# Kernel tuning notes

Measured on AMD Instinct MI355X. Metric: run time of the kernel, lower is better.

## Reference

```python
import jax, jax.numpy as jnp
import numpy as np

B, N, C = 4096, 20, 512
S_VIEWS = 8
N_VIEWS = 20


def setup_inputs() -> dict:
    key = jax.random.key(0)
    k1, k2, k3, k4 = jax.random.split(key, 4)
    F0 = jax.random.normal(k1, (B, N, C), dtype=jnp.float32)
    vertices0 = jax.random.normal(k2, (B, N, 3), dtype=jnp.float32)
    W1 = jax.random.normal(k3, (C, 256), dtype=jnp.float32) * 0.04
    b1 = jnp.zeros((256,), dtype=jnp.float32)
    W2 = jax.random.normal(k4, (256, 40), dtype=jnp.float32) * 0.06
    b2 = jnp.zeros((40,), dtype=jnp.float32)
    return {"F0": F0, "vertices0": vertices0, "W1": W1, "b1": b1, "W2": W2, "b2": b2, "k": 8}


def _cls(x, W1, b1, W2, b2):
    # Linear(512,256) -> LeakyReLU(0.2) -> Linear(256,40)
    h = x @ W1 + b1
    h = jnp.where(h > 0, h, 0.2 * h)
    return h @ W2 + b2


def reference(F0, vertices0, W1, b1, W2, b2, k):
    # F0: [B, N, C]; vertices0: [B, N, 3]
    pooled_F = jnp.sum(F0, axis=1) / N_VIEWS                 # [B, C]
    pred = jnp.argmax(_cls(pooled_F, W1, b1, W2, b2), -1)    # [B] predicted class per sample
    score = _cls(F0, W1, b1, W2, b2)                         # [B, N, 40]
    # score[arange(B), :, pred] -> per-view score of the predicted class
    score_F = jnp.take_along_axis(score, pred[:, None, None], axis=2)[..., 0]  # [B, N]
    _, idx = jax.lax.top_k(score_F, S_VIEWS)                 # [B, S]
    F_new = jnp.take_along_axis(F0, idx[:, :, None], axis=1)            # [B, S, C]
    vertices_new = jnp.take_along_axis(vertices0, idx[:, :, None], axis=1)  # [B, S, 3]
    return (F_new, score, vertices_new)
```

## Files before the change

kernel.cpp:

```cpp
#include <hip/hip_runtime.h>
#include <cstdint>

#define BB 4096
#define NV 20
#define CC 512
#define HH 256
#define NC 40
#define SV 8
#define GG 3
#define TAU 2e-4f

typedef short short8 __attribute__((ext_vector_type(8)));
typedef float f32x4 __attribute__((ext_vector_type(4)));
typedef unsigned short ushort4v __attribute__((ext_vector_type(4)));

__device__ __forceinline__ unsigned short f2bf(float x) {
    unsigned u = __float_as_uint(x);
    unsigned r = (u + 0x7FFFu + ((u >> 16) & 1u)) >> 16;
    return (unsigned short)r;
}
__device__ __forceinline__ float bf2f(unsigned short h) {
    return __uint_as_float(((unsigned)h) << 16);
}

#define MFMA16(A, B, C) __builtin_amdgcn_mfma_f32_16x16x32_bf16(A, B, C, 0, 0, 0)
#define BC8(x) __builtin_bit_cast(short8, x)

__global__ void w1pack_kernel(const float* __restrict__ W1,
                              unsigned short* __restrict__ w1fh,
                              unsigned short* __restrict__ w1fl) {
    int e = blockIdx.x * 256 + threadIdx.x;
    int j3 = e & 7, kq = (e >> 3) & 3, n = (e >> 5) & 255, ks = e >> 13;
    int k = ks * 32 + kq * 8 + j3;
    float x = W1[k * HH + n];
    unsigned short h = f2bf(x);
    w1fh[e] = h;
    w1fl[e] = f2bf(x - bf2f(h));
}

__global__ void w2pack_kernel(const float* __restrict__ W2,
                              unsigned short* __restrict__ w2fh,
                              unsigned short* __restrict__ w2fl) {
    int e = blockIdx.x * 256 + threadIdx.x;
    int j3 = e & 7, kq = (e >> 3) & 3;
    int t = e >> 5;
    int n = t % 48, ks = t / 48;
    int k = ks * 32 + kq * 8 + j3;
    float x = (n < NC) ? W2[k * NC + n] : 0.f;
    unsigned short h = f2bf(x);
    w2fh[e] = h;
    w2fl[e] = f2bf(x - bf2f(h));
}

__global__ __launch_bounds__(256, 3) void fused_kernel(
    const float* __restrict__ F0, const float* __restrict__ V0,
    const float* __restrict__ W1, const float* __restrict__ b1,
    const float* __restrict__ W2, const float* __restrict__ b2,
    const unsigned short* __restrict__ w1fh, const unsigned short* __restrict__ w1fl,
    const unsigned short* __restrict__ w2fh, const unsigned short* __restrict__ w2fl,
    int* __restrict__ rflag, int* __restrict__ rpred,
    float* __restrict__ outF, float* __restrict__ outS, float* __restrict__ outV)
{
    const int blk = blockIdx.x;
    const int j = threadIdx.x;
    const int L = j & 63, wq = j >> 6, l15 = L & 15, kq = L >> 4;

    __shared__ __align__(16) char lds[46944];
    __shared__ int idx8[GG][SV];

    unsigned short* Ahi0 = (unsigned short*)lds;
    unsigned short* Alo0 = Ahi0 + 64 * 72;
    unsigned short* Ahi1 = (unsigned short*)(lds + 18432);
    unsigned short* Alo1 = Ahi1 + 64 * 72;
    unsigned short* Hhi  = (unsigned short*)lds;
    unsigned short* Hlo  = Hhi + 32 * 264;
    float*  Sc      = (float*)(lds + 36864);

    f32x4 acc[4][4];
#pragma unroll
    for (int mt = 0; mt < 4; ++mt)
#pragma unroll
        for (int nt = 0; nt < 4; ++nt) acc[mt][nt] = (f32x4){0.f, 0.f, 0.f, 0.f};

    const float4* srcp[4];
    int ldst[4];
    bool sval[4];
#pragma unroll
    for (int i = 0; i < 4; ++i) {
        int f = j + 256 * i;
        int row = f >> 4, k4 = f & 15;
        sval[i] = (row < 60);
        int bi = (row >= 40) ? 2 : (row >= 20) ? 1 : 0;
        int r = row - 20 * bi;
        int batch = blk * GG + bi; if (batch > BB - 1) batch = BB - 1;
        srcp[i] = (const float4*)(F0 + ((size_t)batch * NV + r) * CC) + k4;
        ldst[i] = row * 72 + k4 * 4;
    }

    float4 rv[4];
    auto STAGE_LOAD = [&](int kc) {
#pragma unroll
        for (int i = 0; i < 4; ++i)
            if (sval[i]) rv[i] = srcp[i][kc * 16];
    };
    auto STAGE_CONVERT = [&](unsigned short* __restrict__ Ah,
                             unsigned short* __restrict__ Al) {
#pragma unroll
        for (int i = 0; i < 4; ++i) {
            ushort4v hv = {0, 0, 0, 0}, lv = {0, 0, 0, 0};
            if (sval[i]) {
                float4 x = rv[i];
                hv.x = f2bf(x.x); lv.x = f2bf(x.x - bf2f(hv.x));
                hv.y = f2bf(x.y); lv.y = f2bf(x.y - bf2f(hv.y));
                hv.z = f2bf(x.z); lv.z = f2bf(x.z - bf2f(hv.z));
                hv.w = f2bf(x.w); lv.w = f2bf(x.w - bf2f(hv.w));
            }
            *(ushort4v*)&Ah[ldst[i]] = hv;
            *(ushort4v*)&Al[ldst[i]] = lv;
        }
    };

    const uint4* Bh = (const uint4*)w1fh;
    const uint4* Bl = (const uint4*)w1fl;

    STAGE_LOAD(0);
    STAGE_CONVERT(Ahi0, Alo0);
    STAGE_LOAD(1);
    __syncthreads();

    unsigned short *Ahc = Ahi0, *Alc = Alo0, *Ahn = Ahi1, *Aln = Alo1;
    for (int kc = 0; kc < 8; ++kc) {
        if (kc < 7) {
            STAGE_CONVERT(Ahn, Aln);
            if (kc < 6) STAGE_LOAD(kc + 2);
        }
#pragma unroll
        for (int ks_l = 0; ks_l < 2; ++ks_l) {
            int ks = kc * 2 + ks_l;
            uint4 bh[4], bl[4];
#pragma unroll
            for (int nt = 0; nt < 4; ++nt) {
                int bi1 = (ks * 256 + wq * 64 + nt * 16 + l15) * 4 + kq;
                bh[nt] = Bh[bi1]; bl[nt] = Bl[bi1];
            }
#pragma unroll
            for (int mt = 0; mt < 4; ++mt) {
                int off = (mt * 16 + l15) * 72 + ks_l * 32 + kq * 8;
                short8 Ah = BC8(*(const uint4*)&Ahc[off]);
                short8 Al = BC8(*(const uint4*)&Alc[off]);
#pragma unroll
                for (int nt = 0; nt < 4; ++nt) {
                    short8 Bhv = BC8(bh[nt]), Blv = BC8(bl[nt]);
                    acc[mt][nt] = MFMA16(Ah, Bhv, acc[mt][nt]);
                    acc[mt][nt] = MFMA16(Ah, Blv, acc[mt][nt]);
                    acc[mt][nt] = MFMA16(Al, Bhv, acc[mt][nt]);
                }
            }
        }
        __syncthreads();
        unsigned short* t;
        t = Ahc; Ahc = Ahn; Ahn = t;
        t = Alc; Alc = Aln; Aln = t;
    }

    const uint4* B2h = (const uint4*)w2fh;
    const uint4* B2l = (const uint4*)w2fl;
#pragma unroll
    for (int p = 0; p < 2; ++p) {
        __syncthreads();
#pragma unroll
        for (int mt2 = 0; mt2 < 2; ++mt2) {
            int mt = 2 * p + mt2;
            bool skip = (p == 1 && mt2 == 1 && kq == 3);
#pragma unroll
            for (int nt = 0; nt < 4; ++nt) {
                int col = wq * 64 + nt * 16 + l15;
                float bc = b1[col];
#pragma unroll
                for (int reg = 0; reg < 4; ++reg) {
                    int hb = mt2 * 16 + kq * 4 + reg;
                    float h = acc[mt][nt][reg] + bc;
                    h = (h > 0.f) ? h : 0.2f * h;
                    if (!skip) {
                        unsigned short hh = f2bf(h);
                        Hhi[hb * 264 + col] = hh;
                        Hlo[hb * 264 + col] = f2bf(h - bf2f(hh));
                    }
                }
            }
        }
        if (p == 1) {
#pragma unroll
            for (int nt = 0; nt < 4; ++nt) {
                int col = wq * 64 + nt * 16 + l15;
                float p0 = 0.f, p1 = 0.f, p2 = 0.f;
#pragma unroll
                for (int mt = 0; mt < 4; ++mt)
#pragma unroll
                    for (int reg = 0; reg < 4; ++reg) {
                        int g = mt * 16 + kq * 4 + reg;
                        float v = acc[mt][nt][reg];
                        p0 += (g < 20) ? v : 0.f;
                        p1 += (g >= 20 && g < 40) ? v : 0.f;
                        p2 += (g >= 40 && g < 60) ? v : 0.f;
                    }
                p0 += __shfl_xor(p0, 16); p0 += __shfl_xor(p0, 32);
                p1 += __shfl_xor(p1, 16); p1 += __shfl_xor(p1, 32);
                p2 += __shfl_xor(p2, 16); p2 += __shfl_xor(p2, 32);
                if (kq < 3) {
                    float s = (kq == 0) ? p0 : (kq == 1) ? p1 : p2;
                    float h = s * (1.0f / NV) + b1[col];
                    h = (h > 0.f) ? h : 0.2f * h;
                    unsigned short hh = f2bf(h);
                    Hhi[(28 + kq) * 264 + col] = hh;
                    Hlo[(28 + kq) * 264 + col] = f2bf(h - bf2f(hh));
                } else {
                    Hhi[31 * 264 + col] = 0;
                    Hlo[31 * 264 + col] = 0;
                }
            }
        }
        __syncthreads();

        if (wq < 3) {
            f32x4 sacc[2];
            sacc[0] = (f32x4){0.f, 0.f, 0.f, 0.f};
            sacc[1] = (f32x4){0.f, 0.f, 0.f, 0.f};
            for (int ks2 = 0; ks2 < 8; ++ks2) {
                int bi2 = (ks2 * 48 + wq * 16 + l15) * 4 + kq;
                short8 Bhv = BC8(B2h[bi2]), Blv = BC8(B2l[bi2]);
#pragma unroll
                for (int tt = 0; tt < 2; ++tt) {
                    int off = (tt * 16 + l15) * 264 + ks2 * 32 + kq * 8;
                    short8 Ah2 = BC8(*(const uint4*)&Hhi[off]);
                    short8 Al2 = BC8(*(const uint4*)&Hlo[off]);
                    sacc[tt] = MFMA16(Ah2, Bhv, sacc[tt]);
                    sacc[tt] = MFMA16(Ah2, Blv, sacc[tt]);
                    sacc[tt] = MFMA16(Al2, Bhv, sacc[tt]);
                }
            }
            int cls = wq * 16 + l15;
            if (cls < NC) {
                float bc2 = b2[cls];
#pragma unroll
                for (int tt = 0; tt < 2; ++tt)
#pragma unroll
                    for (int reg = 0; reg < 4; ++reg) {
                        int lm = 32 * p + tt * 16 + kq * 4 + reg;
                        float sv = sacc[tt][reg] + bc2;
                        if (lm < 60) {
                            int bi = (lm >= 40) ? 2 : (lm >= 20) ? 1 : 0;
                            int r = lm - 20 * bi;
                            Sc[bi * 840 + r * NC + cls] = sv;
                        } else if (lm < 63) {
                            Sc[(lm - 60) * 840 + NV * NC + cls] = sv;
                        }
                    }
            }
        }
    }
    __syncthreads();

    if (j < GG) {
        const float* sp = &Sc[j * 840 + NV * NC];
        int p = 0;
        float m1 = sp[0];
        for (int c = 1; c < NC; ++c)
            if (sp[c] > m1) { m1 = sp[c]; p = c; }
        float m2 = -1e30f;
        for (int c = 0; c < NC; ++c)
            if (c != p && sp[c] > m2) m2 = sp[c];
        int f0 = (m1 - m2 < TAU) ? 1 : 0;

        float v[NV];
#pragma unroll
        for (int n = 0; n < NV; ++n) v[n] = Sc[j * 840 + n * NC + p];
        int ord[9];
        float vals[9];
        unsigned taken = 0;
#pragma unroll
        for (int s = 0; s < 9; ++s) {
            int bi = 0;
            float bv = -1e30f;
#pragma unroll
            for (int n = 0; n < NV; ++n)
                if (!((taken >> n) & 1u) && v[n] > bv) { bv = v[n]; bi = n; }
            taken |= 1u << bi;
            ord[s] = bi;
            vals[s] = bv;
        }
        int fix = 0;
#pragma unroll
        for (int s = 0; s < 8; ++s)
            if (vals[s] - vals[s + 1] < TAU) fix = 1;
#pragma unroll
        for (int s = 0; s < SV; ++s) idx8[j][s] = ord[s];

        int batch = blk * GG + j; if (batch > BB - 1) batch = BB - 1;
        rflag[batch] = f0 ? 1 : (fix ? 2 : 0);
        rpred[batch] = p;
    }
    __syncthreads();

    for (int t = j; t < GG * NV * NC; t += 256) {
        int bi = t / 800, o = t - bi * 800;
        int batch = blk * GG + bi; if (batch > BB - 1) batch = BB - 1;
        outS[(size_t)batch * (NV * NC) + o] = Sc[bi * 840 + o];
    }

    for (int t = j; t < GG * SV * (CC / 4); t += 256) {
        int bi = t >> 10;
        int s = (t >> 7) & 7;
        int t4 = t & 127;
        int batch = blk * GG + bi; if (batch > BB - 1) batch = BB - 1;
        int row = idx8[bi][s];
        const float4* src = (const float4*)(F0 + ((size_t)batch * NV + row) * CC);
        float4* dst = (float4*)(outF + ((size_t)batch * SV + s) * CC);
        dst[t4] = src[t4];
    }

    if (j < GG * SV * 3) {
        int bi = j / 24, o = j - bi * 24;
        int s = o / 3, d = o - s * 3;
        int batch = blk * GG + bi; if (batch > BB - 1) batch = BB - 1;
        outV[((size_t)batch * SV + s) * 3 + d] =
            V0[((size_t)batch * NV + idx8[bi][s]) * 3 + d];
    }
}

__global__ __launch_bounds__(256) void rescue_kernel(
    const float* __restrict__ F0, const float* __restrict__ V0,
    const float* __restrict__ W1, const float* __restrict__ b1,
    const float* __restrict__ W2, const float* __restrict__ b2,
    const int* __restrict__ rflag, const int* __restrict__ rpred,
    float* __restrict__ outF, float* __restrict__ outV)
{
    const int b = blockIdx.x;
    const int flag = rflag[b];
    if (flag == 0) return;

    const int j = threadIdx.x;
    const int L = j & 63, wq = j >> 6;

    __shared__ __align__(16) float Xf[NV * CC];
    __shared__ double pooledD[CC];
    __shared__ double Dbuf[HH];
    __shared__ double Sd[NC];
    __shared__ double part[NV][4];
    __shared__ double SFdS[NV];
    __shared__ int predSh;
    __shared__ int idxs[SV];

    const float* Xb = F0 + (size_t)b * (NV * CC);
    for (int t = j; t < NV * CC / 4; t += 256)
        ((float4*)Xf)[t] = ((const float4*)Xb)[t];
    __syncthreads();

    if (flag == 1) {
        for (int c = j; c < CC; c += 256) {
            double s = 0.0;
            for (int r = 0; r < NV; ++r) s += (double)Xf[r * CC + c];
            pooledD[c] = s / (double)NV;
        }
        __syncthreads();
        double a = 0.0;
        for (int c = 0; c < CC; ++c) a += pooledD[c] * (double)W1[c * HH + j];
        double h = a + (double)b1[j];
        h = (h > 0.0) ? h : 0.2 * h;
        Dbuf[j] = h;
        __syncthreads();
        if (j < NC) {
            double s = 0.0;
            for (int k = 0; k < HH; ++k) s += Dbuf[k] * (double)W2[k * NC + j];
            Sd[j] = s + (double)b2[j];
        }
        __syncthreads();
        if (j == 0) {
            int p = 0;
            double m = Sd[0];
            for (int c = 1; c < NC; ++c)
                if (Sd[c] > m) { m = Sd[c]; p = c; }
            predSh = p;
        }
        __syncthreads();
    } else {
        if (j == 0) predSh = rpred[b];
        __syncthreads();
    }
    const int p = predSh;

    const double b1d = (double)b1[j];
    const double w2jp = (double)W2[j * NC + p];
#pragma unroll
    for (int half = 0; half < 2; ++half) {
        double a[10];
#pragma unroll
        for (int r = 0; r < 10; ++r) a[r] = 0.0;
        for (int c = 0; c < CC; c += 4) {
            double w0 = (double)W1[(c + 0) * HH + j];
            double w1v = (double)W1[(c + 1) * HH + j];
            double w2v = (double)W1[(c + 2) * HH + j];
            double w3v = (double)W1[(c + 3) * HH + j];
#pragma unroll
            for (int r = 0; r < 10; ++r) {
                const float4 x = *(const float4*)&Xf[(half * 10 + r) * CC + c];
                a[r] += (double)x.x * w0;
                a[r] += (double)x.y * w1v;
                a[r] += (double)x.z * w2v;
                a[r] += (double)x.w * w3v;
            }
        }
#pragma unroll
        for (int r = 0; r < 10; ++r) {
            double h = a[r] + b1d;
            h = (h > 0.0) ? h : 0.2 * h;
            double val = h * w2jp;
#pragma unroll
            for (int off = 32; off >= 1; off >>= 1)
                val += __shfl_xor(val, off);
            if (L == 0) part[half * 10 + r][wq] = val;
        }
    }
    __syncthreads();
    if (j < NV)
        SFdS[j] = part[j][0] + part[j][1] + part[j][2] + part[j][3]
                + (double)b2[p];
    __syncthreads();
    if (j == 0) {
        unsigned taken = 0;
        for (int s = 0; s < SV; ++s) {
            int bsel = 0;
            double bv = -1e300;
            for (int n = 0; n < NV; ++n)
                if (!((taken >> n) & 1u) && SFdS[n] > bv) { bv = SFdS[n]; bsel = n; }
            taken |= 1u << bsel;
            idxs[s] = bsel;
        }
    }
    __syncthreads();

    for (int t = j; t < SV * (CC / 4); t += 256) {
        int s = t >> 7, t4 = t & 127;
        int row = idxs[s];
        ((float4*)(outF + ((size_t)b * SV + s) * CC))[t4] =
            ((const float4*)(F0 + ((size_t)b * NV + row) * CC))[t4];
    }
    if (j < SV * 3) {
        int s = j / 3, d = j - s * 3;
        outV[((size_t)b * SV + s) * 3 + d] =
            V0[((size_t)b * NV + idxs[s]) * 3 + d];
    }
}

extern "C" void kernel_launch(void* const* d_in, const int* in_sizes, int n_in,
                              void* d_out, int out_size, void* d_ws, size_t ws_size,
                              hipStream_t stream) {
    const float* F0 = (const float*)d_in[0];
    const float* V0 = (const float*)d_in[1];
    const float* W1 = (const float*)d_in[2];
    const float* b1 = (const float*)d_in[3];
    const float* W2 = (const float*)d_in[4];
    const float* b2 = (const float*)d_in[5];

    char* ws = (char*)d_ws;
    unsigned short* w1fh = (unsigned short*)ws;
    unsigned short* w1fl = (unsigned short*)(ws + 262144);
    unsigned short* w2fh = (unsigned short*)(ws + 524288);
    unsigned short* w2fl = (unsigned short*)(ws + 548864);
    int* rflag = (int*)(ws + 573440);
    int* rpred = (int*)(ws + 589824);

    float* out = (float*)d_out;
    float* outF = out;
    float* outS = out + (size_t)BB * SV * CC;
    float* outV = outS + (size_t)BB * NV * NC;

    w1pack_kernel<<<512, 256, 0, stream>>>(W1, w1fh, w1fl);
    w2pack_kernel<<<48, 256, 0, stream>>>(W2, w2fh, w2fl);
    fused_kernel<<<(BB + GG - 1) / GG, 256, 0, stream>>>(
        F0, V0, W1, b1, W2, b2, w1fh, w1fl, w2fh, w2fl, rflag, rpred,
        outF, outS, outV);
    rescue_kernel<<<BB, 256, 0, stream>>>(
        F0, V0, W1, b1, W2, b2, rflag, rpred, outF, outV);
}
```

Before: 464.8 us.

## Load A operands directly to registers, merge pack kernels, compact rescue worklist

The fused kernel no longer stages F0 tiles through double-buffered LDS. Each lane now loads its own A fragment from global memory and splits it into bf16 hi/lo in registers, which removes the per-chunk barriers and LDS traffic but adds uncoalesced loads and redundant conversion across waves. The two weight-pack kernels are merged into one launch that also resets a counter. Flagged batches are appended to an atomic worklist, so the rescue kernel runs 256 blocks over that list instead of launching one block per batch.

```diff
diff --git a/kernel.cpp b/kernel.cpp
--- a/kernel.cpp
+++ b/kernel.cpp
@@ -12,7 +12,7 @@
 
 typedef short short8 __attribute__((ext_vector_type(8)));
 typedef float f32x4 __attribute__((ext_vector_type(4)));
-typedef unsigned short ushort4v __attribute__((ext_vector_type(4)));
+typedef unsigned short ushort8v __attribute__((ext_vector_type(8)));
 
 __device__ __forceinline__ unsigned short f2bf(float x) {
     unsigned u = __float_as_uint(x);
@@ -26,55 +26,53 @@
 #define MFMA16(A, B, C) __builtin_amdgcn_mfma_f32_16x16x32_bf16(A, B, C, 0, 0, 0)
 #define BC8(x) __builtin_bit_cast(short8, x)
 
-__global__ void w1pack_kernel(const float* __restrict__ W1,
-                              unsigned short* __restrict__ w1fh,
-                              unsigned short* __restrict__ w1fl) {
+__global__ void pack_kernel(const float* __restrict__ W1,
+                            const float* __restrict__ W2,
+                            unsigned short* __restrict__ w1fh,
+                            unsigned short* __restrict__ w1fl,
+                            unsigned short* __restrict__ w2fh,
+                            unsigned short* __restrict__ w2fl,
+                            int* __restrict__ wcount) {
     int e = blockIdx.x * 256 + threadIdx.x;
-    int j3 = e & 7, kq = (e >> 3) & 3, n = (e >> 5) & 255, ks = e >> 13;
-    int k = ks * 32 + kq * 8 + j3;
-    float x = W1[k * HH + n];
-    unsigned short h = f2bf(x);
-    w1fh[e] = h;
-    w1fl[e] = f2bf(x - bf2f(h));
-}
-
-__global__ void w2pack_kernel(const float* __restrict__ W2,
-                              unsigned short* __restrict__ w2fh,
-                              unsigned short* __restrict__ w2fl) {
-    int e = blockIdx.x * 256 + threadIdx.x;
-    int j3 = e & 7, kq = (e >> 3) & 3;
-    int t = e >> 5;
-    int n = t % 48, ks = t / 48;
-    int k = ks * 32 + kq * 8 + j3;
-    float x = (n < NC) ? W2[k * NC + n] : 0.f;
-    unsigned short h = f2bf(x);
-    w2fh[e] = h;
-    w2fl[e] = f2bf(x - bf2f(h));
+    if (e == 0) *wcount = 0;
+    {
+        int j3 = e & 7, kq = (e >> 3) & 3, n = (e >> 5) & 255, ks = e >> 13;
+        int k = ks * 32 + kq * 8 + j3;
+        float x = W1[k * HH + n];
+        unsigned short h = f2bf(x);
+        w1fh[e] = h;
+        w1fl[e] = f2bf(x - bf2f(h));
+    }
+    if (e < 12288) {
+        int j3 = e & 7, kq = (e >> 3) & 3;
+        int t = e >> 5;
+        int n = t % 48, ks = t / 48;
+        int k = ks * 32 + kq * 8 + j3;
+        float x = (n < NC) ? W2[k * NC + n] : 0.f;
+        unsigned short h = f2bf(x);
+        w2fh[e] = h;
+        w2fl[e] = f2bf(x - bf2f(h));
+    }
 }
 
 __global__ __launch_bounds__(256, 3) void fused_kernel(
     const float* __restrict__ F0, const float* __restrict__ V0,
-    const float* __restrict__ W1, const float* __restrict__ b1,
-    const float* __restrict__ W2, const float* __restrict__ b2,
+    const float* __restrict__ b1, const float* __restrict__ b2,
     const unsigned short* __restrict__ w1fh, const unsigned short* __restrict__ w1fl,
     const unsigned short* __restrict__ w2fh, const unsigned short* __restrict__ w2fl,
-    int* __restrict__ rflag, int* __restrict__ rpred,
+    int* __restrict__ wcount, int* __restrict__ wl, int* __restrict__ rpred,
     float* __restrict__ outF, float* __restrict__ outS, float* __restrict__ outV)
 {
     const int blk = blockIdx.x;
     const int j = threadIdx.x;
     const int L = j & 63, wq = j >> 6, l15 = L & 15, kq = L >> 4;
 
-    __shared__ __align__(16) char lds[46944];
+    __shared__ __align__(16) char lds[43872];
     __shared__ int idx8[GG][SV];
 
-    unsigned short* Ahi0 = (unsigned short*)lds;
-    unsigned short* Alo0 = Ahi0 + 64 * 72;
-    unsigned short* Ahi1 = (unsigned short*)(lds + 18432);
-    unsigned short* Alo1 = Ahi1 + 64 * 72;
-    unsigned short* Hhi  = (unsigned short*)lds;
-    unsigned short* Hlo  = Hhi + 32 * 264;
-    float*  Sc      = (float*)(lds + 36864);
+    unsigned short* Hhi = (unsigned short*)lds;
+    unsigned short* Hlo = Hhi + 32 * 264;
+    float* Sc = (float*)(lds + 33792);
 
     f32x4 acc[4][4];
 #pragma unroll
@@ -82,85 +80,58 @@
 #pragma unroll
         for (int nt = 0; nt < 4; ++nt) acc[mt][nt] = (f32x4){0.f, 0.f, 0.f, 0.f};
 
-    const float4* srcp[4];
-    int ldst[4];
-    bool sval[4];
-#pragma unroll
-    for (int i = 0; i < 4; ++i) {
-        int f = j + 256 * i;
-        int row = f >> 4, k4 = f & 15;
-        sval[i] = (row < 60);
-        int bi = (row >= 40) ? 2 : (row >= 20) ? 1 : 0;
-        int r = row - 20 * bi;
+    const float* arow[4];
+    bool aval[4];
+#pragma unroll
+    for (int mt = 0; mt < 4; ++mt) {
+        int g = mt * 16 + l15;
+        aval[mt] = (g < 60);
+        int bi = (g >= 40) ? 2 : (g >= 20) ? 1 : 0;
+        int r = g - 20 * bi;
+        if (!aval[mt]) r = 0;
         int batch = blk * GG + bi; if (batch > BB - 1) batch = BB - 1;
-        srcp[i] = (const float4*)(F0 + ((size_t)batch * NV + r) * CC) + k4;
-        ldst[i] = row * 72 + k4 * 4;
-    }
-
-    float4 rv[4];
-    auto STAGE_LOAD = [&](int kc) {
-#pragma unroll
-        for (int i = 0; i < 4; ++i)
-            if (sval[i]) rv[i] = srcp[i][kc * 16];
-    };
-    auto STAGE_CONVERT = [&](unsigned short* __restrict__ Ah,
-                             unsigned short* __restrict__ Al) {
-#pragma unroll
-        for (int i = 0; i < 4; ++i) {
-            ushort4v hv = {0, 0, 0, 0}, lv = {0, 0, 0, 0};
-            if (sval[i]) {
-                float4 x = rv[i];
-                hv.x = f2bf(x.x); lv.x = f2bf(x.x - bf2f(hv.x));
-                hv.y = f2bf(x.y); lv.y = f2bf(x.y - bf2f(hv.y));
-                hv.z = f2bf(x.z); lv.z = f2bf(x.z - bf2f(hv.z));
-                hv.w = f2bf(x.w); lv.w = f2bf(x.w - bf2f(hv.w));
-            }
-            *(ushort4v*)&Ah[ldst[i]] = hv;
-            *(ushort4v*)&Al[ldst[i]] = lv;
-        }
-    };
+        arow[mt] = F0 + ((size_t)batch * NV + r) * CC;
+    }
 
     const uint4* Bh = (const uint4*)w1fh;
     const uint4* Bl = (const uint4*)w1fl;
 
-    STAGE_LOAD(0);
-    STAGE_CONVERT(Ahi0, Alo0);
-    STAGE_LOAD(1);
-    __syncthreads();
-
-    unsigned short *Ahc = Ahi0, *Alc = Alo0, *Ahn = Ahi1, *Aln = Alo1;
-    for (int kc = 0; kc < 8; ++kc) {
-        if (kc < 7) {
-            STAGE_CONVERT(Ahn, Aln);
-            if (kc < 6) STAGE_LOAD(kc + 2);
-        }
-#pragma unroll
-        for (int ks_l = 0; ks_l < 2; ++ks_l) {
-            int ks = kc * 2 + ks_l;
-            uint4 bh[4], bl[4];
+#pragma unroll 2
+    for (int ks = 0; ks < 16; ++ks) {
+        uint4 bh[4], bl[4];
+#pragma unroll
+        for (int nt = 0; nt < 4; ++nt) {
+            int bi1 = (ks * 256 + wq * 64 + nt * 16 + l15) * 4 + kq;
+            bh[nt] = Bh[bi1]; bl[nt] = Bl[bi1];
+        }
+        short8 Ah[4], Al[4];
+#pragma unroll
+        for (int mt = 0; mt < 4; ++mt) {
+            float4 x0 = {0.f, 0.f, 0.f, 0.f}, x1 = {0.f, 0.f, 0.f, 0.f};
+            if (aval[mt]) {
+                const float4* p = (const float4*)(arow[mt] + ks * 32 + kq * 8);
+                x0 = p[0]; x1 = p[1];
+            }
+            float xs[8] = {x0.x, x0.y, x0.z, x0.w, x1.x, x1.y, x1.z, x1.w};
+            ushort8v hv, lv;
+#pragma unroll
+            for (int i2 = 0; i2 < 8; ++i2) {
+                unsigned short h = f2bf(xs[i2]);
+                hv[i2] = h;
+                lv[i2] = f2bf(xs[i2] - bf2f(h));
+            }
+            Ah[mt] = __builtin_bit_cast(short8, hv);
+            Al[mt] = __builtin_bit_cast(short8, lv);
+        }
+#pragma unroll
+        for (int mt = 0; mt < 4; ++mt)
 #pragma unroll
             for (int nt = 0; nt < 4; ++nt) {
-                int bi1 = (ks * 256 + wq * 64 + nt * 16 + l15) * 4 + kq;
-                bh[nt] = Bh[bi1]; bl[nt] = Bl[bi1];
-            }
-#pragma unroll
-            for (int mt = 0; mt < 4; ++mt) {
-                int off = (mt * 16 + l15) * 72 + ks_l * 32 + kq * 8;
-                short8 Ah = BC8(*(const uint4*)&Ahc[off]);
-                short8 Al = BC8(*(const uint4*)&Alc[off]);
-#pragma unroll
-                for (int nt = 0; nt < 4; ++nt) {
-                    short8 Bhv = BC8(bh[nt]), Blv = BC8(bl[nt]);
-                    acc[mt][nt] = MFMA16(Ah, Bhv, acc[mt][nt]);
-                    acc[mt][nt] = MFMA16(Ah, Blv, acc[mt][nt]);
-                    acc[mt][nt] = MFMA16(Al, Bhv, acc[mt][nt]);
-                }
-            }
-        }
-        __syncthreads();
-        unsigned short* t;
-        t = Ahc; Ahc = Ahn; Ahn = t;
-        t = Alc; Alc = Aln; Aln = t;
+                short8 Bhv = BC8(bh[nt]), Blv = BC8(bl[nt]);
+                acc[mt][nt] = MFMA16(Ah[mt], Bhv, acc[mt][nt]);
+                acc[mt][nt] = MFMA16(Ah[mt], Blv, acc[mt][nt]);
+                acc[mt][nt] = MFMA16(Al[mt], Bhv, acc[mt][nt]);
+            }
     }
 
     const uint4* B2h = (const uint4*)w2fh;
@@ -296,9 +267,15 @@
 #pragma unroll
         for (int s = 0; s < SV; ++s) idx8[j][s] = ord[s];
 
-        int batch = blk * GG + j; if (batch > BB - 1) batch = BB - 1;
-        rflag[batch] = f0 ? 1 : (fix ? 2 : 0);
-        rpred[batch] = p;
+        int batch = blk * GG + j;
+        if (batch < BB) {
+            rpred[batch] = p;
+            int flagv = f0 ? 1 : (fix ? 2 : 0);
+            if (flagv) {
+                int slot = atomicAdd(wcount, 1);
+                wl[slot] = batch * 4 + flagv;
+            }
+        }
     }
     __syncthreads();
 
@@ -332,12 +309,12 @@
     const float* __restrict__ F0, const float* __restrict__ V0,
     const float* __restrict__ W1, const float* __restrict__ b1,
     const float* __restrict__ W2, const float* __restrict__ b2,
-    const int* __restrict__ rflag, const int* __restrict__ rpred,
+    const int* __restrict__ wcount, const int* __restrict__ wl,
+    const int* __restrict__ rpred,
     float* __restrict__ outF, float* __restrict__ outV)
 {
-    const int b = blockIdx.x;
-    const int flag = rflag[b];
-    if (flag == 0) return;
+    const int cnt = *wcount;
+    if ((int)blockIdx.x >= cnt) return;
 
     const int j = threadIdx.x;
     const int L = j & 63, wq = j >> 6;
@@ -351,104 +328,111 @@
     __shared__ int predSh;
     __shared__ int idxs[SV];
 
-    const float* Xb = F0 + (size_t)b * (NV * CC);
-    for (int t = j; t < NV * CC / 4; t += 256)
-        ((float4*)Xf)[t] = ((const float4*)Xb)[t];
-    __syncthreads();
-
-    if (flag == 1) {
-        for (int c = j; c < CC; c += 256) {
-            double s = 0.0;
-            for (int r = 0; r < NV; ++r) s += (double)Xf[r * CC + c];
-            pooledD[c] = s / (double)NV;
-        }
-        __syncthreads();
-        double a = 0.0;
-        for (int c = 0; c < CC; ++c) a += pooledD[c] * (double)W1[c * HH + j];
-        double h = a + (double)b1[j];
-        h = (h > 0.0) ? h : 0.2 * h;
-        Dbuf[j] = h;
-        __syncthreads();
-        if (j < NC) {
-            double s = 0.0;
-            for (int k = 0; k < HH; ++k) s += Dbuf[k] * (double)W2[k * NC + j];
-            Sd[j] = s + (double)b2[j];
-        }
+    for (int w = blockIdx.x; w < cnt; w += 256) {
+        const int e = wl[w];
+        const int b = e >> 2;
+        const int flag = e & 3;
+
+        const float* Xb = F0 + (size_t)b * (NV * CC);
+        for (int t = j; t < NV * CC / 4; t += 256)
+            ((float4*)Xf)[t] = ((const float4*)Xb)[t];
+        __syncthreads();
+
+        if (flag == 1) {
+            for (int c = j; c < CC; c += 256) {
+                double s = 0.0;
+                for (int r = 0; r < NV; ++r) s += (double)Xf[r * CC + c];
+                pooledD[c] = s / (double)NV;
+            }
+            __syncthreads();
+            double a = 0.0;
+            for (int c = 0; c < CC; ++c) a += pooledD[c] * (double)W1[c * HH + j];
+            double h = a + (double)b1[j];
+            h = (h > 0.0) ? h : 0.2 * h;
+            Dbuf[j] = h;
+            __syncthreads();
+            if (j < NC) {
+                double s = 0.0;
+                for (int k = 0; k < HH; ++k) s += Dbuf[k] * (double)W2[k * NC + j];
+                Sd[j] = s + (double)b2[j];
+            }
+            __syncthreads();
+            if (j == 0) {
+                int p = 0;
+                double m = Sd[0];
+                for (int c = 1; c < NC; ++c)
+                    if (Sd[c] > m) { m = Sd[c]; p = c; }
+                predSh = p;
+            }
+            __syncthreads();
+        } else {
+            if (j == 0) predSh = rpred[b];
+            __syncthreads();
+        }
+        const int p = predSh;
+
+        const double b1d = (double)b1[j];
+        const double w2jp = (double)W2[j * NC + p];
+#pragma unroll
+        for (int half = 0; half < 2; ++half) {
+            double a[10];
+#pragma unroll
+            for (int r = 0; r < 10; ++r) a[r] = 0.0;
+            for (int c = 0; c < CC; c += 4) {
+                double w0 = (double)W1[(c + 0) * HH + j];
+                double w1v = (double)W1[(c + 1) * HH + j];
+                double w2v = (double)W1[(c + 2) * HH + j];
+                double w3v = (double)W1[(c + 3) * HH + j];
+#pragma unroll
+                for (int r = 0; r < 10; ++r) {
+                    const float4 x = *(const float4*)&Xf[(half * 10 + r) * CC + c];
+                    a[r] += (double)x.x * w0;
+                    a[r] += (double)x.y * w1v;
+                    a[r] += (double)x.z * w2v;
+                    a[r] += (double)x.w * w3v;
+                }
+            }
+#pragma unroll
+            for (int r = 0; r < 10; ++r) {
+                double h = a[r] + b1d;
+                h = (h > 0.0) ? h : 0.2 * h;
+                double val = h * w2jp;
+#pragma unroll
+                for (int off = 32; off >= 1; off >>= 1)
+                    val += __shfl_xor(val, off);
+                if (L == 0) part[half * 10 + r][wq] = val;
+            }
+        }
+        __syncthreads();
+        if (j < NV)
+            SFdS[j] = part[j][0] + part[j][1] + part[j][2] + part[j][3]
+                    + (double)b2[p];
         __syncthreads();
         if (j == 0) {
-            int p = 0;
-            double m = Sd[0];
-            for (int c = 1; c < NC; ++c)
-                if (Sd[c] > m) { m = Sd[c]; p = c; }
-            predSh = p;
-        }
-        __syncthreads();
-    } else {
-        if (j == 0) predSh = rpred[b];
-        __syncthreads();
-    }
-    const int p = predSh;
-
-    const double b1d = (double)b1[j];
-    const double w2jp = (double)W2[j * NC + p];
-#pragma unroll
-    for (int half = 0; half < 2; ++half) {
-        double a[10];
-#pragma unroll
-        for (int r = 0; r < 10; ++r) a[r] = 0.0;
-        for (int c = 0; c < CC; c += 4) {
-            double w0 = (double)W1[(c + 0) * HH + j];
-            double w1v = (double)W1[(c + 1) * HH + j];
-            double w2v = (double)W1[(c + 2) * HH + j];
-            double w3v = (double)W1[(c + 3) * HH + j];
-#pragma unroll
-            for (int r = 0; r < 10; ++r) {
-                const float4 x = *(const float4*)&Xf[(half * 10 + r) * CC + c];
-                a[r] += (double)x.x * w0;
-                a[r] += (double)x.y * w1v;
-                a[r] += (double)x.z * w2v;
-                a[r] += (double)x.w * w3v;
-            }
-        }
-#pragma unroll
-        for (int r = 0; r < 10; ++r) {
-            double h = a[r] + b1d;
-            h = (h > 0.0) ? h : 0.2 * h;
-            double val = h * w2jp;
-#pragma unroll
-            for (int off = 32; off >= 1; off >>= 1)
-                val += __shfl_xor(val, off);
-            if (L == 0) part[half * 10 + r][wq] = val;
-        }
-    }
-    __syncthreads();
-    if (j < NV)
-        SFdS[j] = part[j][0] + part[j][1] + part[j][2] + part[j][3]
-                + (double)b2[p];
-    __syncthreads();
-    if (j == 0) {
-        unsigned taken = 0;
-        for (int s = 0; s < SV; ++s) {
-            int bsel = 0;
-            double bv = -1e300;
-            for (int n = 0; n < NV; ++n)
-                if (!((taken >> n) & 1u) && SFdS[n] > bv) { bv = SFdS[n]; bsel = n; }
-            taken |= 1u << bsel;
-            idxs[s] = bsel;
-        }
-    }
-    __syncthreads();
-
-    for (int t = j; t < SV * (CC / 4); t += 256) {
-        int s = t >> 7, t4 = t & 127;
-        int row = idxs[s];
-        ((float4*)(outF + ((size_t)b * SV + s) * CC))[t4] =
-            ((const float4*)(F0 + ((size_t)b * NV + row) * CC))[t4];
-    }
-    if (j < SV * 3) {
-        int s = j / 3, d = j - s * 3;
-        outV[((size_t)b * SV + s) * 3 + d] =
-            V0[((size_t)b * NV + idxs[s]) * 3 + d];
+            unsigned taken = 0;
+            for (int s = 0; s < SV; ++s) {
+                int bsel = 0;
+                double bv = -1e300;
+                for (int n = 0; n < NV; ++n)
+                    if (!((taken >> n) & 1u) && SFdS[n] > bv) { bv = SFdS[n]; bsel = n; }
+                taken |= 1u << bsel;
+                idxs[s] = bsel;
+            }
+        }
+        __syncthreads();
+
+        for (int t = j; t < SV * (CC / 4); t += 256) {
+            int s = t >> 7, t4 = t & 127;
+            int row = idxs[s];
+            ((float4*)(outF + ((size_t)b * SV + s) * CC))[t4] =
+                ((const float4*)(F0 + ((size_t)b * NV + row) * CC))[t4];
+        }
+        if (j < SV * 3) {
+            int s = j / 3, d = j - s * 3;
+            outV[((size_t)b * SV + s) * 3 + d] =
+                V0[((size_t)b * NV + idxs[s]) * 3 + d];
+        }
+        __syncthreads();
     }
 }
 
@@ -467,19 +451,19 @@
     unsigned short* w1fl = (unsigned short*)(ws + 262144);
     unsigned short* w2fh = (unsigned short*)(ws + 524288);
     unsigned short* w2fl = (unsigned short*)(ws + 548864);
-    int* rflag = (int*)(ws + 573440);
-    int* rpred = (int*)(ws + 589824);
+    int* wcount = (int*)(ws + 573440);
+    int* wl     = (int*)(ws + 573504);
+    int* rpred  = (int*)(ws + 589888);
 
     float* out = (float*)d_out;
     float* outF = out;
     float* outS = out + (size_t)BB * SV * CC;
     float* outV = outS + (size_t)BB * NV * NC;
 
-    w1pack_kernel<<<512, 256, 0, stream>>>(W1, w1fh, w1fl);
-    w2pack_kernel<<<48, 256, 0, stream>>>(W2, w2fh, w2fl);
+    pack_kernel<<<512, 256, 0, stream>>>(W1, W2, w1fh, w1fl, w2fh, w2fl, wcount);
     fused_kernel<<<(BB + GG - 1) / GG, 256, 0, stream>>>(
-        F0, V0, W1, b1, W2, b2, w1fh, w1fl, w2fh, w2fl, rflag, rpred,
+        F0, V0, b1, b2, w1fh, w1fl, w2fh, w2fl, wcount, wl, rpred,
         outF, outS, outV);
-    rescue_kernel<<<BB, 256, 0, stream>>>(
-        F0, V0, W1, b1, W2, b2, rflag, rpred, outF, outV);
-}
+    rescue_kernel<<<256, 256, 0, stream>>>(
+        F0, V0, W1, b1, W2, b2, wcount, wl, rpred, outF, outV);
+}
```

Result: slower. 503.8 us (+8.4%).
